# Optimization experiments

Measured on AMD Instinct MI355X. Metric: run time of the kernel, lower is better.

## Reference

```python
import jax, jax.numpy as jnp
import numpy as np

B, C, H, W = 4, 256, 64, 64
CI = C // 2
EPS = 1e-5


def setup_inputs() -> dict:
    key = jax.random.key(0)
    ks = jax.random.split(key, 3)
    return {
        "x": jax.random.normal(ks[0], (B, C, H, W), dtype=jnp.float32) * 0.1,
        "g_w": jax.random.normal(ks[1], (CI, C), dtype=jnp.float32) * 0.05,
        "g_b": jnp.zeros((CI,), dtype=jnp.float32),
        "W_w": jax.random.normal(ks[2], (C, CI), dtype=jnp.float32) * 0.05,
        "W_b": jnp.zeros((C,), dtype=jnp.float32),
        "gamma": jnp.ones((C,), dtype=jnp.float32),
        "beta": jnp.zeros((C,), dtype=jnp.float32),
    }


def reference(x, g_w, g_b, W_w, W_b, gamma, beta):
    b, c, h, w = x.shape
    n = h * w
    ci = g_w.shape[0]
    # g: 1x1 conv C -> C/2
    g_x = jnp.einsum('oc,bchw->bohw', g_w, x) + g_b[None, :, None, None]
    g_x = g_x.reshape(b, ci, n).transpose(0, 2, 1)          # [B, N, Ci]
    theta = x.reshape(b, c, n).transpose(0, 2, 1)           # [B, N, C]
    phi = x.reshape(b, c, n)                                # [B, C, N]
    f = jnp.einsum('bnc,bcm->bnm', theta, phi)              # [B, N, N]
    attn = jax.nn.softmax(f, axis=-1)
    y = jnp.einsum('bnm,bmc->bnc', attn, g_x)               # [B, N, Ci]
    y = y.transpose(0, 2, 1).reshape(b, ci, h, w)
    # W: 1x1 conv C/2 -> C, then BatchNorm2d (training-mode batch stats)
    wy = jnp.einsum('oc,bchw->bohw', W_w, y) + W_b[None, :, None, None]
    mean = wy.mean(axis=(0, 2, 3))
    var = wy.var(axis=(0, 2, 3))  # biased, as torch BN uses for normalization
    wy = (wy - mean[None, :, None, None]) * jax.lax.rsqrt(var[None, :, None, None] + EPS)
    wy = wy * gamma[None, :, None, None] + beta[None, :, None, None]
    return wy + x
```

## Files before the change

kernel.cpp:

```cpp
#include <hip/hip_runtime.h>
#include <math.h>

#define B_ 4
#define C_ 256
#define CI_ 128
#define N_ 4096
#define QT_ 128
#define KT_ 64
#define KH_ 2048
#define NITER (KH_ / KT_)
#define KSTRIDE 264
#define VSTRIDE 72
constexpr float EPS_ = 1e-5f;

typedef __attribute__((ext_vector_type(8))) short bfrag;
typedef __attribute__((ext_vector_type(4))) float f4;
typedef __attribute__((ext_vector_type(16))) float facc16;

__device__ __forceinline__ unsigned short bf16r(float x) {
    unsigned u = __float_as_uint(x);
    u += 0x7FFFu + ((u >> 16) & 1u);
    return (unsigned short)(u >> 16);
}
__device__ __forceinline__ unsigned pack_bf16(float a, float b) {
    unsigned ua = __float_as_uint(a); ua += 0x7FFFu + ((ua >> 16) & 1u);
    unsigned ub = __float_as_uint(b); ub += 0x7FFFu + ((ub >> 16) & 1u);
    return (ua >> 16) | (ub & 0xFFFF0000u);
}

__global__ __launch_bounds__(256) void make_xt(const float* __restrict__ x,
                                               unsigned short* __restrict__ xt,
                                               float* __restrict__ sums) {
    if (blockIdx.x == 0 && blockIdx.y == 0 && blockIdx.z == 0) {
        sums[threadIdx.x] = 0.f;
        sums[threadIdx.x + 256] = 0.f;
    }
    int n  = blockIdx.x * 256 + threadIdx.x;
    int c0 = blockIdx.y * 8;
    int b  = blockIdx.z;
    const float* xb = x + (size_t)b * C_ * N_;
    unsigned short buf[8];
#pragma unroll
    for (int c = 0; c < 8; c++) buf[c] = bf16r(xb[(c0 + c) * N_ + n]);
    uint4 v;
    v.x = buf[0] | ((unsigned)buf[1] << 16);
    v.y = buf[2] | ((unsigned)buf[3] << 16);
    v.z = buf[4] | ((unsigned)buf[5] << 16);
    v.w = buf[6] | ((unsigned)buf[7] << 16);
    *(uint4*)&xt[((size_t)b * N_ + n) * C_ + c0] = v;
}

__global__ __launch_bounds__(256) void gconv(const float* __restrict__ x,
                                             const float* __restrict__ gw,
                                             const float* __restrict__ gb,
                                             unsigned short* __restrict__ gx) {
    int m  = blockIdx.x * 256 + threadIdx.x;
    int o0 = blockIdx.y * 16;
    int b  = blockIdx.z;
    const float* xb = x + (size_t)b * C_ * N_;
    float acc[16];
#pragma unroll
    for (int o = 0; o < 16; o++) acc[o] = gb[o0 + o];
    for (int c0 = 0; c0 < C_; c0 += 8) {
        float xv[8];
#pragma unroll
        for (int j = 0; j < 8; j++) xv[j] = xb[(c0 + j) * N_ + m];
#pragma unroll
        for (int o = 0; o < 16; o++) {
            const float* wr = gw + (size_t)(o0 + o) * C_ + c0;
#pragma unroll
            for (int j = 0; j < 8; j++) acc[o] += wr[j] * xv[j];
        }
    }
#pragma unroll
    for (int o = 0; o < 16; o++)
        gx[((size_t)b * CI_ + o0 + o) * N_ + m] = bf16r(acc[o]);
}

__global__ __launch_bounds__(512, 2) void attn(const unsigned short* __restrict__ xt,
                                               const unsigned short* __restrict__ gx,
                                               float* __restrict__ Yp,
                                               float* __restrict__ ml) {
    __shared__ __align__(16) unsigned short Ks[2][64 * KSTRIDE];
    __shared__ __align__(16) unsigned short Vs[2][128 * VSTRIDE];
    __shared__ __align__(16) unsigned short Ps[128 * VSTRIDE];

    const int tid  = threadIdx.x;
    const int lane = tid & 63, w = tid >> 6;
    const int wq = w & 3, g = w >> 2;
    const int col = lane & 31, h = lane >> 5;
    const int half = blockIdx.x & 1;
    const int b    = (blockIdx.x & 7) >> 1;
    const int qt   = blockIdx.x >> 3;
    const int n0   = qt * QT_;
    const int kbase = half * KH_;
    const unsigned short* xtb = xt + (size_t)b * N_ * C_;
    const unsigned short* gxb = gx + (size_t)b * CI_ * N_;

    bfrag qb[16];
#pragma unroll
    for (int kc = 0; kc < 16; kc++)
        qb[kc] = *(const bfrag*)(xtb + (size_t)(n0 + 32 * wq + col) * C_ + kc * 16 + h * 8);

    facc16 yacc[4];
#pragma unroll
    for (int t = 0; t < 4; t++)
#pragma unroll
        for (int r = 0; r < 16; r++) yacc[t][r] = 0.f;
    float mrun = -INFINITY, lrun = 0.f;

    uint4 kreg[4], vreg[2];
#pragma unroll
    for (int r = 0; r < 4; r++) {
        int idx = r * 512 + tid;
        kreg[r] = *(const uint4*)(xtb + (size_t)(kbase + (idx >> 5)) * C_ + (idx & 31) * 8);
    }
#pragma unroll
    for (int r = 0; r < 2; r++) {
        int idx = r * 512 + tid;
        vreg[r] = *(const uint4*)(gxb + (size_t)(idx >> 3) * N_ + kbase + (idx & 7) * 8);
    }
#pragma unroll
    for (int r = 0; r < 4; r++) {
        int idx = r * 512 + tid;
        *(uint4*)&Ks[0][(idx >> 5) * KSTRIDE + (idx & 31) * 8] = kreg[r];
    }
#pragma unroll
    for (int r = 0; r < 2; r++) {
        int idx = r * 512 + tid;
        *(uint4*)&Vs[0][(idx >> 3) * VSTRIDE + (idx & 7) * 8] = vreg[r];
    }
#pragma unroll
    for (int r = 0; r < 4; r++) {
        int idx = r * 512 + tid;
        kreg[r] = *(const uint4*)(xtb + (size_t)(kbase + KT_ + (idx >> 5)) * C_ + (idx & 31) * 8);
    }
#pragma unroll
    for (int r = 0; r < 2; r++) {
        int idx = r * 512 + tid;
        vreg[r] = *(const uint4*)(gxb + (size_t)(idx >> 3) * N_ + kbase + KT_ + (idx & 7) * 8);
    }
    __syncthreads();

    for (int it = 0; it < NITER; ++it) {
        const int cur = it & 1, nxt = cur ^ 1;

        if (it + 1 < NITER) {
#pragma unroll
            for (int r = 0; r < 4; r++) {
                int idx = r * 512 + tid;
                *(uint4*)&Ks[nxt][(idx >> 5) * KSTRIDE + (idx & 31) * 8] = kreg[r];
            }
#pragma unroll
            for (int r = 0; r < 2; r++) {
                int idx = r * 512 + tid;
                *(uint4*)&Vs[nxt][(idx >> 3) * VSTRIDE + (idx & 7) * 8] = vreg[r];
            }
        }
        if (it + 2 < NITER) {
            const int t0 = kbase + (it + 2) * KT_;
#pragma unroll
            for (int r = 0; r < 4; r++) {
                int idx = r * 512 + tid;
                kreg[r] = *(const uint4*)(xtb + (size_t)(t0 + (idx >> 5)) * C_ + (idx & 31) * 8);
            }
#pragma unroll
            for (int r = 0; r < 2; r++) {
                int idx = r * 512 + tid;
                vreg[r] = *(const uint4*)(gxb + (size_t)(idx >> 3) * N_ + t0 + (idx & 7) * 8);
            }
        }

        facc16 sa, sb;
#pragma unroll
        for (int r = 0; r < 16; r++) { sa[r] = 0.f; sb[r] = 0.f; }
#pragma unroll
        for (int kc = 0; kc < 8; kc++) {
            bfrag ka0 = *(const bfrag*)&Ks[cur][(32 * g + col) * KSTRIDE + (2 * kc) * 16 + h * 8];
            bfrag ka1 = *(const bfrag*)&Ks[cur][(32 * g + col) * KSTRIDE + (2 * kc + 1) * 16 + h * 8];
            sa = __builtin_amdgcn_mfma_f32_32x32x16_bf16(ka0, qb[2 * kc], sa, 0, 0, 0);
            sb = __builtin_amdgcn_mfma_f32_32x32x16_bf16(ka1, qb[2 * kc + 1], sb, 0, 0, 0);
        }
        facc16 sacc = sa + sb;

        float mx = -INFINITY;
#pragma unroll
        for (int r = 0; r < 16; r++) mx = fmaxf(mx, sacc[r]);
        mx = fmaxf(mx, __shfl_xor(mx, 32, 64));
        float mn = fmaxf(mrun, mx);
        float alpha = __expf(mrun - mn);
        mrun = mn;
        lrun *= alpha;
        if (__any(alpha != 1.f)) {
#pragma unroll
            for (int t = 0; t < 4; t++)
#pragma unroll
                for (int r = 0; r < 16; r++) yacc[t][r] *= alpha;
        }

        {
            const int q = 32 * wq + col;
            float lsum = 0.f;
#pragma unroll
            for (int r = 0; r < 16; r++) {
                sacc[r] = __expf(sacc[r] - mrun);
                lsum += sacc[r];
            }
            lrun += lsum;
#pragma unroll
            for (int rq = 0; rq < 4; rq++) {
                unsigned lo = pack_bf16(sacc[4 * rq + 0], sacc[4 * rq + 1]);
                unsigned hi = pack_bf16(sacc[4 * rq + 2], sacc[4 * rq + 3]);
                unsigned long long pv = (unsigned long long)lo
                                      | ((unsigned long long)hi << 32);
                *(unsigned long long*)&Ps[q * VSTRIDE + 32 * g + 8 * rq + 4 * h] = pv;
            }
        }

#pragma unroll
        for (int mc = 0; mc < 2; mc++) {
            bfrag pb = *(const bfrag*)&Ps[(32 * wq + col) * VSTRIDE + 32 * g + mc * 16 + h * 8];
#pragma unroll
            for (int ct = 0; ct < 4; ct++) {
                bfrag va = *(const bfrag*)&Vs[cur][(32 * ct + col) * VSTRIDE + 32 * g + mc * 16 + h * 8];
                yacc[ct] = __builtin_amdgcn_mfma_f32_32x32x16_bf16(va, pb, yacc[ct], 0, 0, 0);
            }
        }

        __syncthreads();
    }

    lrun += __shfl_xor(lrun, 32, 64);

    float* PsF = (float*)Ps;
    float* Ysc = PsF;
    float* mlb = PsF + 4096;

    const int q = 32 * wq + col;
    if (h == 0) {
        mlb[(g * 128 + q) * 2]     = mrun;
        mlb[(g * 128 + q) * 2 + 1] = lrun;
    }
    __syncthreads();
    float m0 = mlb[q * 2],           l0 = mlb[q * 2 + 1];
    float m1 = mlb[(128 + q) * 2],   l1 = mlb[(128 + q) * 2 + 1];
    float mm = fmaxf(m0, m1);
    float e0 = __expf(m0 - mm), e1 = __expf(m1 - mm);
    float lnew = e0 * l0 + e1 * l1;

#pragma unroll
    for (int ct = 0; ct < 4; ct++) {
        if (g == 1) {
#pragma unroll
            for (int r = 0; r < 16; r++) {
                int cl = (r & 3) + 8 * (r >> 2) + 4 * h;
                Ysc[cl * 128 + q] = e1 * yacc[ct][r];
            }
        }
        __syncthreads();
        if (g == 0) {
#pragma unroll
            for (int r = 0; r < 16; r++) {
                int cl = (r & 3) + 8 * (r >> 2) + 4 * h;
                float v = e0 * yacc[ct][r] + Ysc[cl * 128 + q];
                Yp[(((size_t)half * 4 + b) * CI_ + 32 * ct + cl) * N_ + n0 + q] = v;
            }
        }
        __syncthreads();
    }
    if (g == 0 && h == 0) {
        ml[(((size_t)half * 4 + b) * N_ + n0 + q) * 2]     = mm;
        ml[(((size_t)half * 4 + b) * N_ + n0 + q) * 2 + 1] = lnew;
    }
}

__global__ __launch_bounds__(256) void merge(const float* __restrict__ Yp,
                                             const float* __restrict__ ml,
                                             float* __restrict__ y) {
    int n4 = blockIdx.x * 256 + threadIdx.x;
    int ci = blockIdx.y;
    int b  = blockIdx.z;
    int n  = n4 * 4;
    float4 a0 = *(const float4*)&ml[((size_t)b * N_ + n) * 2];
    float4 a1 = *(const float4*)&ml[((size_t)b * N_ + n + 2) * 2];
    float4 c0 = *(const float4*)&ml[(((size_t)4 + b) * N_ + n) * 2];
    float4 c1 = *(const float4*)&ml[(((size_t)4 + b) * N_ + n + 2) * 2];
    float m0[4] = {a0.x, a0.z, a1.x, a1.z};
    float l0[4] = {a0.y, a0.w, a1.y, a1.w};
    float m1[4] = {c0.x, c0.z, c1.x, c1.z};
    float l1[4] = {c0.y, c0.w, c1.y, c1.w};
    float w0[4], w1[4];
#pragma unroll
    for (int k = 0; k < 4; k++) {
        float mm = fmaxf(m0[k], m1[k]);
        float e0 = __expf(m0[k] - mm), e1 = __expf(m1[k] - mm);
        float inv = 1.f / (e0 * l0[k] + e1 * l1[k]);
        w0[k] = e0 * inv;
        w1[k] = e1 * inv;
    }
    size_t base = ((size_t)b * CI_ + ci) * N_ + n;
    float4 y0 = *(const float4*)&Yp[base];
    float4 y1 = *(const float4*)&Yp[(size_t)4 * CI_ * N_ + base];
    float4 o;
    o.x = w0[0] * y0.x + w1[0] * y1.x;
    o.y = w0[1] * y0.y + w1[1] * y1.y;
    o.z = w0[2] * y0.z + w1[2] * y1.z;
    o.w = w0[3] * y0.w + w1[3] * y1.w;
    *(float4*)&y[base] = o;
}

__global__ __launch_bounds__(256) void wconv_stats(const float* __restrict__ y,
                                                   const float* __restrict__ Ww,
                                                   const float* __restrict__ Wb,
                                                   float* __restrict__ wy,
                                                   float* __restrict__ sums) {
    int n   = blockIdx.x * 256 + threadIdx.x;
    int co0 = blockIdx.y * 16;
    int b   = blockIdx.z;
    const float* yb = y + (size_t)b * CI_ * N_;
    float acc[16];
#pragma unroll
    for (int o = 0; o < 16; o++) acc[o] = Wb[co0 + o];
    for (int c0 = 0; c0 < CI_; c0 += 8) {
        float yv[8];
#pragma unroll
        for (int j = 0; j < 8; j++) yv[j] = yb[(c0 + j) * N_ + n];
#pragma unroll
        for (int o = 0; o < 16; o++) {
            const float* wr = Ww + (size_t)(co0 + o) * CI_ + c0;
#pragma unroll
            for (int j = 0; j < 8; j++) acc[o] += wr[j] * yv[j];
        }
    }
    float* wyb = wy + (size_t)b * C_ * N_;
#pragma unroll
    for (int o = 0; o < 16; o++) wyb[(co0 + o) * N_ + n] = acc[o];

    __shared__ float wred[32][4];
    int lane = threadIdx.x & 63, wid = threadIdx.x >> 6;
#pragma unroll
    for (int o = 0; o < 16; o++) {
        float s1 = acc[o], s2 = acc[o] * acc[o];
#pragma unroll
        for (int off = 32; off > 0; off >>= 1) {
            s1 += __shfl_down(s1, off, 64);
            s2 += __shfl_down(s2, off, 64);
        }
        if (lane == 0) { wred[o][wid] = s1; wred[16 + o][wid] = s2; }
    }
    __syncthreads();
    if (threadIdx.x < 32) {
        int qq = threadIdx.x;
        float t = wred[qq][0] + wred[qq][1] + wred[qq][2] + wred[qq][3];
        int o = qq & 15;
        if (qq < 16) atomicAdd(&sums[co0 + o], t);
        else         atomicAdd(&sums[256 + co0 + o], t);
    }
}

__global__ __launch_bounds__(256) void bn_finalize(float* __restrict__ wy,
                                                   const float* __restrict__ x,
                                                   const float* __restrict__ sums,
                                                   const float* __restrict__ gamma,
                                                   const float* __restrict__ beta,
                                                   float* __restrict__ out) {
    int n4 = blockIdx.x * 256 + threadIdx.x;
    int co = blockIdx.y;
    int b  = blockIdx.z;
    float cnt  = (float)(B_ * N_);
    float mean = sums[co] / cnt;
    float var  = sums[256 + co] / cnt - mean * mean;
    float sc   = rsqrtf(var + EPS_) * gamma[co];
    float bt   = beta[co];
    size_t idx = ((size_t)b * C_ + co) * N_ + (size_t)n4 * 4;
    float4 wv = *(const float4*)&wy[idx];
    float4 xv = *(const float4*)&x[idx];
    float4 o;
    o.x = (wv.x - mean) * sc + bt + xv.x;
    o.y = (wv.y - mean) * sc + bt + xv.y;
    o.z = (wv.z - mean) * sc + bt + xv.z;
    o.w = (wv.w - mean) * sc + bt + xv.w;
    *(float4*)&out[idx] = o;
}

extern "C" void kernel_launch(void* const* d_in, const int* in_sizes, int n_in,
                              void* d_out, int out_size, void* d_ws, size_t ws_size,
                              hipStream_t stream) {
    const float* x     = (const float*)d_in[0];
    const float* gw    = (const float*)d_in[1];
    const float* gb    = (const float*)d_in[2];
    const float* Ww    = (const float*)d_in[3];
    const float* Wb    = (const float*)d_in[4];
    const float* gamma = (const float*)d_in[5];
    const float* beta  = (const float*)d_in[6];
    float* out = (float*)d_out;
    float* ws  = (float*)d_ws;

    unsigned short* xt  = (unsigned short*)ws;
    unsigned short* gxb = (unsigned short*)(ws + 2097152);
    float* Yp   = ws + 3145728;
    float* ml   = ws + 7340032;
    float* sums = ws + 7405568;
    float* y    = ws;
    float* wy   = out;

    hipLaunchKernelGGL(make_xt, dim3(16, 32, 4), dim3(256), 0, stream, x, xt, sums);
    hipLaunchKernelGGL(gconv, dim3(16, 8, 4), dim3(256), 0, stream, x, gw, gb, gxb);
    hipLaunchKernelGGL(attn, dim3(256), dim3(512), 0, stream, xt, gxb, Yp, ml);
    hipLaunchKernelGGL(merge, dim3(4, 128, 4), dim3(256), 0, stream, Yp, ml, y);
    hipLaunchKernelGGL(wconv_stats, dim3(16, 16, 4), dim3(256), 0, stream, y, Ww, Wb, wy, sums);
    hipLaunchKernelGGL(bn_finalize, dim3(4, 256, 4), dim3(256), 0, stream, wy, x, sums, gamma, beta, out);
}
```

Measured before the change: 280.4 us.

## Software-pipeline PV matmul one step behind QK and swizzle LDS layouts

Restructures the attention loop so the P·V MFMAs for the previous key tile run right after the current QK^T MFMAs, overlapping softmax with matrix work. This uses a triple-buffered V, a double-buffered P and one barrier per iteration instead of a store-then-read on the same P buffer. Padded LDS strides are replaced by XOR-swizzled layouts to avoid bank conflicts, and MFMA sections get raised wave priority. The max is now rescaled lazily, only when it grows by more than 8, which skips rescale work but lets exponents reach up to e^8 before renormalizing.

```diff
diff --git a/kernel.cpp b/kernel.cpp
--- a/kernel.cpp
+++ b/kernel.cpp
@@ -9,8 +9,6 @@
 #define KT_ 64
 #define KH_ 2048
 #define NITER (KH_ / KT_)
-#define KSTRIDE 264
-#define VSTRIDE 72
 constexpr float EPS_ = 1e-5f;
 
 typedef __attribute__((ext_vector_type(8))) short bfrag;
@@ -81,14 +79,15 @@
                                                const unsigned short* __restrict__ gx,
                                                float* __restrict__ Yp,
                                                float* __restrict__ ml) {
-    __shared__ __align__(16) unsigned short Ks[2][64 * KSTRIDE];
-    __shared__ __align__(16) unsigned short Vs[2][128 * VSTRIDE];
-    __shared__ __align__(16) unsigned short Ps[128 * VSTRIDE];
+    __shared__ __align__(16) unsigned short Ks[2][64 * 256];
+    __shared__ __align__(16) unsigned short Vs[3][128 * 64];
+    __shared__ __align__(16) unsigned short Ps[2][128 * 64];
 
     const int tid  = threadIdx.x;
     const int lane = tid & 63, w = tid >> 6;
     const int wq = w & 3, g = w >> 2;
     const int col = lane & 31, h = lane >> 5;
+    const int c7 = col & 7;
     const int half = blockIdx.x & 1;
     const int b    = (blockIdx.x & 7) >> 1;
     const int qt   = blockIdx.x >> 3;
@@ -107,7 +106,7 @@
     for (int t = 0; t < 4; t++)
 #pragma unroll
         for (int r = 0; r < 16; r++) yacc[t][r] = 0.f;
-    float mrun = -INFINITY, lrun = 0.f;
+    float mrun = -INFINITY, lrun = 0.f, aprev = 1.f;
 
     uint4 kreg[4], vreg[2];
 #pragma unroll
@@ -123,12 +122,14 @@
 #pragma unroll
     for (int r = 0; r < 4; r++) {
         int idx = r * 512 + tid;
-        *(uint4*)&Ks[0][(idx >> 5) * KSTRIDE + (idx & 31) * 8] = kreg[r];
+        int row = idx >> 5, gr = idx & 31;
+        *(uint4*)&Ks[0][row * 256 + ((gr ^ (row & 31)) << 3)] = kreg[r];
     }
 #pragma unroll
     for (int r = 0; r < 2; r++) {
         int idx = r * 512 + tid;
-        *(uint4*)&Vs[0][(idx >> 3) * VSTRIDE + (idx & 7) * 8] = vreg[r];
+        int row = idx >> 3, gr = idx & 7;
+        *(uint4*)&Vs[0][row * 64 + ((gr ^ (row & 7)) << 3)] = vreg[r];
     }
 #pragma unroll
     for (int r = 0; r < 4; r++) {
@@ -146,15 +147,18 @@
         const int cur = it & 1, nxt = cur ^ 1;
 
         if (it + 1 < NITER) {
+            const int vb = (it + 1) % 3;
 #pragma unroll
             for (int r = 0; r < 4; r++) {
                 int idx = r * 512 + tid;
-                *(uint4*)&Ks[nxt][(idx >> 5) * KSTRIDE + (idx & 31) * 8] = kreg[r];
+                int row = idx >> 5, gr = idx & 31;
+                *(uint4*)&Ks[nxt][row * 256 + ((gr ^ (row & 31)) << 3)] = kreg[r];
             }
 #pragma unroll
             for (int r = 0; r < 2; r++) {
                 int idx = r * 512 + tid;
-                *(uint4*)&Vs[nxt][(idx >> 3) * VSTRIDE + (idx & 7) * 8] = vreg[r];
+                int row = idx >> 3, gr = idx & 7;
+                *(uint4*)&Vs[vb][row * 64 + ((gr ^ (row & 7)) << 3)] = vreg[r];
             }
         }
         if (it + 2 < NITER) {
@@ -171,31 +175,54 @@
             }
         }
 
+        __builtin_amdgcn_s_setprio(1);
         facc16 sa, sb;
 #pragma unroll
         for (int r = 0; r < 16; r++) { sa[r] = 0.f; sb[r] = 0.f; }
-#pragma unroll
-        for (int kc = 0; kc < 8; kc++) {
-            bfrag ka0 = *(const bfrag*)&Ks[cur][(32 * g + col) * KSTRIDE + (2 * kc) * 16 + h * 8];
-            bfrag ka1 = *(const bfrag*)&Ks[cur][(32 * g + col) * KSTRIDE + (2 * kc + 1) * 16 + h * 8];
-            sa = __builtin_amdgcn_mfma_f32_32x32x16_bf16(ka0, qb[2 * kc], sa, 0, 0, 0);
-            sb = __builtin_amdgcn_mfma_f32_32x32x16_bf16(ka1, qb[2 * kc + 1], sb, 0, 0, 0);
-        }
+        {
+            const unsigned short* krow = &Ks[cur][(32 * g + col) * 256];
+#pragma unroll
+            for (int kc = 0; kc < 8; kc++) {
+                bfrag ka0 = *(const bfrag*)&krow[(((4 * kc + h) ^ col)) << 3];
+                bfrag ka1 = *(const bfrag*)&krow[(((4 * kc + 2 + h) ^ col)) << 3];
+                sa = __builtin_amdgcn_mfma_f32_32x32x16_bf16(ka0, qb[2 * kc], sa, 0, 0, 0);
+                sb = __builtin_amdgcn_mfma_f32_32x32x16_bf16(ka1, qb[2 * kc + 1], sb, 0, 0, 0);
+            }
+        }
+        if (it > 0) {
+            if (__any(aprev != 1.f)) {
+#pragma unroll
+                for (int t = 0; t < 4; t++)
+#pragma unroll
+                    for (int r = 0; r < 16; r++) yacc[t][r] *= aprev;
+            }
+            const int pv = (it - 1) & 1, vb = (it - 1) % 3;
+#pragma unroll
+            for (int mc = 0; mc < 2; mc++) {
+                const int gr = 4 * g + 2 * mc + h;
+                bfrag pb = *(const bfrag*)&Ps[pv][(32 * wq + col) * 64 + ((gr ^ c7) << 3)];
+#pragma unroll
+                for (int ct = 0; ct < 4; ct++) {
+                    bfrag va = *(const bfrag*)&Vs[vb][(32 * ct + col) * 64 + ((gr ^ c7) << 3)];
+                    yacc[ct] = __builtin_amdgcn_mfma_f32_32x32x16_bf16(va, pb, yacc[ct], 0, 0, 0);
+                }
+            }
+        }
+        __builtin_amdgcn_s_setprio(0);
+
         facc16 sacc = sa + sb;
 
         float mx = -INFINITY;
 #pragma unroll
         for (int r = 0; r < 16; r++) mx = fmaxf(mx, sacc[r]);
         mx = fmaxf(mx, __shfl_xor(mx, 32, 64));
-        float mn = fmaxf(mrun, mx);
-        float alpha = __expf(mrun - mn);
-        mrun = mn;
-        lrun *= alpha;
-        if (__any(alpha != 1.f)) {
-#pragma unroll
-            for (int t = 0; t < 4; t++)
-#pragma unroll
-                for (int r = 0; r < 16; r++) yacc[t][r] *= alpha;
+        if (__any(mx > mrun + 8.f)) {
+            float mn = fmaxf(mrun, mx);
+            aprev = __expf(mrun - mn);
+            lrun *= aprev;
+            mrun = mn;
+        } else {
+            aprev = 1.f;
         }
 
         {
@@ -213,28 +240,38 @@
                 unsigned hi = pack_bf16(sacc[4 * rq + 2], sacc[4 * rq + 3]);
                 unsigned long long pv = (unsigned long long)lo
                                       | ((unsigned long long)hi << 32);
-                *(unsigned long long*)&Ps[q * VSTRIDE + 32 * g + 8 * rq + 4 * h] = pv;
-            }
-        }
-
+                *(unsigned long long*)&Ps[cur][q * 64 + (((4 * g + rq) ^ c7) << 3) + 4 * h] = pv;
+            }
+        }
+
+        __syncthreads();
+    }
+
+    if (__any(aprev != 1.f)) {
+#pragma unroll
+        for (int t = 0; t < 4; t++)
+#pragma unroll
+            for (int r = 0; r < 16; r++) yacc[t][r] *= aprev;
+    }
+    {
+        const int pv = (NITER - 1) & 1, vb = (NITER - 1) % 3;
 #pragma unroll
         for (int mc = 0; mc < 2; mc++) {
-            bfrag pb = *(const bfrag*)&Ps[(32 * wq + col) * VSTRIDE + 32 * g + mc * 16 + h * 8];
+            const int gr = 4 * g + 2 * mc + h;
+            bfrag pb = *(const bfrag*)&Ps[pv][(32 * wq + col) * 64 + ((gr ^ c7) << 3)];
 #pragma unroll
             for (int ct = 0; ct < 4; ct++) {
-                bfrag va = *(const bfrag*)&Vs[cur][(32 * ct + col) * VSTRIDE + 32 * g + mc * 16 + h * 8];
+                bfrag va = *(const bfrag*)&Vs[vb][(32 * ct + col) * 64 + ((gr ^ c7) << 3)];
                 yacc[ct] = __builtin_amdgcn_mfma_f32_32x32x16_bf16(va, pb, yacc[ct], 0, 0, 0);
             }
         }
-
-        __syncthreads();
     }
 
     lrun += __shfl_xor(lrun, 32, 64);
 
-    float* PsF = (float*)Ps;
-    float* Ysc = PsF;
-    float* mlb = PsF + 4096;
+    float* KsF = (float*)Ks;
+    float* Ysc = KsF;
+    float* mlb = KsF + 4096;
 
     const int q = 32 * wq + col;
     if (h == 0) {
```

New measurement: 308.8 us. 1.1x slower.
